# Performance work log

Measured on AMD Instinct MI355X. Metric: run time of the kernel, lower is better.

The kernel has to match this reference:

```python
import jax, jax.numpy as jnp
import numpy as np

IN_FT = 256
OUT_FT = 256


def setup_inputs() -> dict:
    key = jax.random.key(0)
    k1, k2, k3 = jax.random.split(key, 3)
    B, N = 4, 4096
    seq = jax.random.normal(k1, (B, N, IN_FT), dtype=jnp.float32)
    adj = jax.random.uniform(k2, (B, N, N), dtype=jnp.float32)
    # Xavier-uniform fc weight [out_ft, in_ft], bias zeros
    limit = float(np.sqrt(6.0 / (IN_FT + OUT_FT)))
    W = jax.random.uniform(k3, (OUT_FT, IN_FT), minval=-limit, maxval=limit, dtype=jnp.float32)
    b = jnp.zeros((OUT_FT,), dtype=jnp.float32)
    alpha = jnp.array(0.25, dtype=jnp.float32)  # PReLU shared parameter
    return {"seq": seq, "adj": adj, "W": W, "b": b, "alpha": alpha}


def reference(seq, adj, W, b, alpha):
    # Linear projection: [B, N, out_ft]
    h = jnp.einsum("bni,oi->bno", seq, W) + b
    # Neighbor aggregation (dense bmm path): [B, N, N] @ [B, N, out_ft]
    h = jnp.einsum("bnm,bmo->bno", adj, h)
    # PReLU with shared alpha
    return jnp.where(h > 0, h, alpha * h)
```

## Files before the change

### kernel.cpp

```cpp
#include <hip/hip_runtime.h>
#include <hip/hip_bf16.h>

#define NSEQ 4096
#define FT 256
#define BK 64
#define BKB 128
#define NTB (NSEQ / BKB)

typedef __attribute__((ext_vector_type(8))) short bf16x8;
typedef __attribute__((ext_vector_type(4))) float f32x4;

__device__ __forceinline__ ushort f2bf(float f) {
  __hip_bfloat16 h = __float2bfloat16(f);
  return *reinterpret_cast<const ushort*>(&h);
}

__device__ __forceinline__ int swz(int row, int byteInRow) {
  return row * 128 + (byteInRow ^ ((row & 7) << 4));
}

__device__ __forceinline__ void mma_step(const char* lAp, const char* lBp,
                                         int lane, int wm, int wn,
                                         f32x4 acc[2][4]) {
  const int r16 = lane & 15;
  const int g16 = (lane >> 4) * 16;
#pragma unroll
  for (int kk = 0; kk < 2; ++kk) {
    const int kb = kk * 64 + g16;
    bf16x8 a[2], b[4];
#pragma unroll
    for (int mi = 0; mi < 2; ++mi) {
      const int row = wm * 32 + mi * 16 + r16;
      a[mi] = *reinterpret_cast<const bf16x8*>(lAp + swz(row, kb));
    }
#pragma unroll
    for (int ni = 0; ni < 4; ++ni) {
      const int row = wn * 64 + ni * 16 + r16;
      b[ni] = *reinterpret_cast<const bf16x8*>(lBp + swz(row, kb));
    }
#pragma unroll
    for (int mi = 0; mi < 2; ++mi)
#pragma unroll
      for (int ni = 0; ni < 4; ++ni)
        acc[mi][ni] = __builtin_amdgcn_mfma_f32_16x16x32_bf16(a[mi], b[ni],
                                                             acc[mi][ni], 0, 0, 0);
  }
}

__global__ __launch_bounds__(512) void linear_kernel(
    const float* __restrict__ seq, const float* __restrict__ W,
    const float* __restrict__ bias, ushort* __restrict__ hT) {
  __shared__ __align__(16) ushort lA[2][64 * 64];
  __shared__ __align__(16) ushort lB[2][256 * 64];

  const int tid = threadIdx.x;
  const int lane = tid & 63;
  const int wid = tid >> 6;
  const int wm = wid >> 2, wn = wid & 3;
  const int m0 = blockIdx.x * 64;

  const int ar = tid >> 4, ac = tid & 15;

  f32x4 rA[2];
  f32x4 rB[8];

  auto gload = [&](int t) {
    const int k0 = t * BK;
#pragma unroll
    for (int p = 0; p < 2; ++p)
      rA[p] = *reinterpret_cast<const f32x4*>(
          seq + (size_t)(m0 + ar + p * 32) * FT + k0 + ac * 4);
#pragma unroll
    for (int p = 0; p < 8; ++p)
      rB[p] = *reinterpret_cast<const f32x4*>(
          W + (size_t)(ar + p * 32) * FT + k0 + ac * 4);
  };
  auto lwrite = [&](int buf) {
    char* lAp = (char*)lA[buf];
    char* lBp = (char*)lB[buf];
#pragma unroll
    for (int p = 0; p < 2; ++p) {
      ushort4 u = make_ushort4(f2bf(rA[p][0]), f2bf(rA[p][1]), f2bf(rA[p][2]), f2bf(rA[p][3]));
      *reinterpret_cast<ushort4*>(lAp + swz(ar + p * 32, ac * 8)) = u;
    }
#pragma unroll
    for (int p = 0; p < 8; ++p) {
      ushort4 u = make_ushort4(f2bf(rB[p][0]), f2bf(rB[p][1]), f2bf(rB[p][2]), f2bf(rB[p][3]));
      *reinterpret_cast<ushort4*>(lBp + swz(ar + p * 32, ac * 8)) = u;
    }
  };

  f32x4 acc[2][4];
  const f32x4 zero = {0.f, 0.f, 0.f, 0.f};
#pragma unroll
  for (int mi = 0; mi < 2; ++mi)
#pragma unroll
    for (int ni = 0; ni < 4; ++ni) acc[mi][ni] = zero;

  gload(0);
  lwrite(0);
  const int NTA = FT / BK;
  for (int t = 0; t < NTA; ++t) {
    const int cur = t & 1;
    __syncthreads();
    if (t + 1 < NTA) gload(t + 1);
    mma_step((const char*)lA[cur], (const char*)lB[cur], lane, wm, wn, acc);
    if (t + 1 < NTA) lwrite(cur ^ 1);
  }

#pragma unroll
  for (int mi = 0; mi < 2; ++mi) {
    const int grow = m0 + wm * 32 + mi * 16 + ((lane >> 4) << 2);
    const int batch = grow >> 12;
    const int n = grow & (NSEQ - 1);
#pragma unroll
    for (int ni = 0; ni < 4; ++ni) {
      const int o = wn * 64 + ni * 16 + (lane & 15);
      const float bo = bias[o];
      ushort4 u;
      u.x = f2bf(acc[mi][ni][0] + bo);
      u.y = f2bf(acc[mi][ni][1] + bo);
      u.z = f2bf(acc[mi][ni][2] + bo);
      u.w = f2bf(acc[mi][ni][3] + bo);
      *reinterpret_cast<ushort4*>(hT + (size_t)(batch * FT + o) * NSEQ + n) = u;
    }
  }
}

__global__ __launch_bounds__(512) void bmm_prelu_kernel(
    const float* __restrict__ adj, const ushort* __restrict__ hT,
    const float* __restrict__ alphaP, float* __restrict__ out) {
  __shared__ __align__(16) char smem[2 * 65536 + 2 * 16384];

  const int tid = threadIdx.x;
  const int lane = tid & 63;
  const int wid = tid >> 6;
  const int wm = wid >> 2, wn = wid & 3;

  const int bid = blockIdx.x;
  const int sbid = (bid & 7) * 32 + (bid >> 3);
  const int batch = sbid >> 6;
  const int m0 = (sbid & 63) * 64;

  const float* adjB = adj + (size_t)batch * NSEQ * NSEQ + (size_t)m0 * NSEQ;
  const ushort* hTB = hT + (size_t)batch * FT * NSEQ;

  auto lB = [&](int i) -> char* { return smem + i * 65536; };
  auto lA = [&](int i) -> char* { return smem + 131072 + i * 16384; };

  const int arow = tid >> 3, ac = tid & 7;
  const int bro = (lane >> 4);
  const int bhalf = (lane >> 3) & 1;
  f32x4 rS[4];

  f32x4 acc[2][4];
  const f32x4 zero = {0.f, 0.f, 0.f, 0.f};
#pragma unroll
  for (int mi = 0; mi < 2; ++mi)
#pragma unroll
    for (int ni = 0; ni < 4; ++ni) acc[mi][ni] = zero;

  auto issueA = [&](int t) {
    const int k0 = t * BKB;
#pragma unroll
    for (int q = 0; q < 4; ++q)
      rS[q] = *reinterpret_cast<const f32x4*>(
          adjB + (size_t)arow * NSEQ + k0 + ac * 16 + q * 4);
  };
  auto issueB = [&](int t, int ib) {
    const int k0 = t * BKB;
#pragma unroll
    for (int p = 0; p < 8; ++p) {
      const int grow = wid * 32 + p * 4 + bro;
      const int gsrc = (lane & 7) ^ (((p & 1) * 4 + bro) & 7);
      const ushort* gp = hTB + (size_t)grow * NSEQ + k0 + bhalf * 64 + gsrc * 8;
      char* lp = lB(ib) + wid * 8192 + p * 1024;
      __builtin_amdgcn_global_load_lds(
          (const __attribute__((address_space(1))) void*)gp,
          (__attribute__((address_space(3))) void*)lp, 16, 0, 0);
    }
  };
  auto writeA = [&](int ia) {
    char* lAp = lA(ia);
    const int half = ac >> 2;
#pragma unroll
    for (int q = 0; q < 4; ++q) {
      ushort4 u = make_ushort4(f2bf(rS[q][0]), f2bf(rS[q][1]),
                               f2bf(rS[q][2]), f2bf(rS[q][3]));
      const int gih = (((ac & 3) * 2 + (q >> 1)) ^ (arow & 7));
      *reinterpret_cast<ushort4*>(lAp + arow * 256 + half * 128 + gih * 16 +
                                  (q & 1) * 8) = u;
    }
  };
  auto mma32 = [&](const char* lAp, const char* lBp) {
    const int r16 = lane & 15;
    const int sub = lane >> 4;
#pragma unroll
    for (int kk = 0; kk < 4; ++kk) {
      const int half = kk >> 1;
      const int gih = (((kk & 1) * 4 + sub) ^ (r16 & 7));
      const int bofs = half * 128 + gih * 16;
      bf16x8 a[2], b[4];
#pragma unroll
      for (int mi = 0; mi < 2; ++mi) {
        const int row = wm * 32 + mi * 16 + r16;
        a[mi] = *reinterpret_cast<const bf16x8*>(lAp + row * 256 + bofs);
      }
#pragma unroll
      for (int ni = 0; ni < 4; ++ni) {
        const int row = wn * 64 + ni * 16 + r16;
        b[ni] = *reinterpret_cast<const bf16x8*>(lBp + row * 256 + bofs);
      }
#pragma unroll
      for (int mi = 0; mi < 2; ++mi)
#pragma unroll
        for (int ni = 0; ni < 4; ++ni)
          acc[mi][ni] = __builtin_amdgcn_mfma_f32_16x16x32_bf16(
              a[mi], b[ni], acc[mi][ni], 0, 0, 0);
    }
  };

  issueA(0);
  __builtin_amdgcn_sched_barrier(0);
  issueB(0, 0);
  __builtin_amdgcn_sched_barrier(0);
  asm volatile("s_waitcnt vmcnt(8)" ::: "memory");
  __builtin_amdgcn_sched_barrier(0);
  writeA(0);
  asm volatile("s_waitcnt vmcnt(0) lgkmcnt(0)" ::: "memory");
  __builtin_amdgcn_s_barrier();
  __builtin_amdgcn_sched_barrier(0);

  auto body = [&](int t, int cur) {
    issueA(t + 1);
    __builtin_amdgcn_sched_barrier(0);
    issueB(t + 1, cur ^ 1);
    __builtin_amdgcn_sched_barrier(0);
    __builtin_amdgcn_s_setprio(1);
    mma32(lA(cur), lB(cur));
    __builtin_amdgcn_s_setprio(0);
    asm volatile("s_waitcnt vmcnt(8)" ::: "memory");
    __builtin_amdgcn_sched_barrier(0);
    writeA(cur ^ 1);
    asm volatile("s_waitcnt vmcnt(0) lgkmcnt(0)" ::: "memory");
    __builtin_amdgcn_s_barrier();
    __builtin_amdgcn_sched_barrier(0);
  };

  for (int j = 0; j < 15; ++j) {
    body(2 * j, 0);
    body(2 * j + 1, 1);
  }
  body(30, 0);
  __builtin_amdgcn_s_setprio(1);
  mma32(lA(1), lB(1));
  __builtin_amdgcn_s_setprio(0);

  const float alpha = *alphaP;
  __syncthreads();
  float* lo = (float*)smem;
  const int PITCH = 264;
#pragma unroll
  for (int mi = 0; mi < 2; ++mi) {
    const int rbase = wm * 32 + mi * 16 + ((lane >> 4) << 2);
#pragma unroll
    for (int ni = 0; ni < 4; ++ni) {
      const int o = wn * 64 + ni * 16 + (lane & 15);
#pragma unroll
      for (int j = 0; j < 4; ++j) {
        float v = acc[mi][ni][j];
        v = v > 0.f ? v : alpha * v;
        lo[(rbase + j) * PITCH + o] = v;
      }
    }
  }
  __syncthreads();
  float* outB = out + ((size_t)batch * NSEQ + m0) * FT;
  const int r = tid >> 3, c8 = tid & 7;
#pragma unroll
  for (int k = 0; k < 8; ++k) {
    const int g = c8 + k * 8;
    f32x4 v = *reinterpret_cast<const f32x4*>(lo + r * PITCH + g * 4);
    __builtin_nontemporal_store(v, reinterpret_cast<f32x4*>(outB + (size_t)r * FT + g * 4));
  }
}

extern "C" void kernel_launch(void* const* d_in, const int* in_sizes, int n_in,
                              void* d_out, int out_size, void* d_ws, size_t ws_size,
                              hipStream_t stream) {
  const float* seq = (const float*)d_in[0];
  const float* adj = (const float*)d_in[1];
  const float* W = (const float*)d_in[2];
  const float* bias = (const float*)d_in[3];
  const float* alpha = (const float*)d_in[4];
  float* out = (float*)d_out;
  ushort* hT = (ushort*)d_ws;

  linear_kernel<<<256, 512, 0, stream>>>(seq, W, bias, hT);
  bmm_prelu_kernel<<<256, 512, 0, stream>>>(adj, hT, alpha, out);
}
```

Measured before the change: 83.63 us.

## Split B tile into half-K ring stages with finer-grained load/compute overlap

Replaces the double-buffered 128-wide B tile with a four-slot ring of 64-wide half tiles, so the second half of the next B tile is issued only after the first half of the current compute. Waits now use partial vmcnt counts and an extra mid-iteration barrier, which lets global-to-LDS loads overlap MFMA work more finely and stops draining all loads before each barrier. The B LDS layout changes to 128-byte rows with a new XOR swizzle. The cost is an extra barrier per iteration and reliance on exact waitcnt counts for correctness.

```diff
diff --git a/kernel.cpp b/kernel.cpp
--- a/kernel.cpp
+++ b/kernel.cpp
@@ -130,7 +130,7 @@
 __global__ __launch_bounds__(512) void bmm_prelu_kernel(
     const float* __restrict__ adj, const ushort* __restrict__ hT,
     const float* __restrict__ alphaP, float* __restrict__ out) {
-  __shared__ __align__(16) char smem[2 * 65536 + 2 * 16384];
+  __shared__ __align__(16) char smem[4 * 32768 + 2 * 16384];
 
   const int tid = threadIdx.x;
   const int lane = tid & 63;
@@ -145,12 +145,13 @@
   const float* adjB = adj + (size_t)batch * NSEQ * NSEQ + (size_t)m0 * NSEQ;
   const ushort* hTB = hT + (size_t)batch * FT * NSEQ;
 
-  auto lB = [&](int i) -> char* { return smem + i * 65536; };
+  auto ring = [&](int i) -> char* { return smem + i * 32768; };
   auto lA = [&](int i) -> char* { return smem + 131072 + i * 16384; };
 
+  const int br = lane >> 3;
+  const int bgr = (lane & 7) ^ br;
   const int arow = tid >> 3, ac = tid & 7;
-  const int bro = (lane >> 4);
-  const int bhalf = (lane >> 3) & 1;
+
   f32x4 rS[4];
 
   f32x4 acc[2][4];
@@ -167,14 +168,13 @@
       rS[q] = *reinterpret_cast<const f32x4*>(
           adjB + (size_t)arow * NSEQ + k0 + ac * 16 + q * 4);
   };
-  auto issueB = [&](int t, int ib) {
-    const int k0 = t * BKB;
-#pragma unroll
-    for (int p = 0; p < 8; ++p) {
-      const int grow = wid * 32 + p * 4 + bro;
-      const int gsrc = (lane & 7) ^ (((p & 1) * 4 + bro) & 7);
-      const ushort* gp = hTB + (size_t)grow * NSEQ + k0 + bhalf * 64 + gsrc * 8;
-      char* lp = lB(ib) + wid * 8192 + p * 1024;
+  auto issueBh = [&](int t, int h, int s) {
+    const int k0 = t * BKB + h * 64;
+#pragma unroll
+    for (int p = 0; p < 4; ++p) {
+      const ushort* gp =
+          hTB + (size_t)(p * 64 + wid * 8 + br) * NSEQ + k0 + bgr * 8;
+      char* lp = ring(s) + p * 8192 + wid * 1024;
       __builtin_amdgcn_global_load_lds(
           (const __attribute__((address_space(1))) void*)gp,
           (__attribute__((address_space(3))) void*)lp, 16, 0, 0);
@@ -192,25 +192,21 @@
                                   (q & 1) * 8) = u;
     }
   };
-  auto mma32 = [&](const char* lAp, const char* lBp) {
+  auto compute_half = [&](int h, const char* lAp, const char* lBp) {
     const int r16 = lane & 15;
     const int sub = lane >> 4;
 #pragma unroll
-    for (int kk = 0; kk < 4; ++kk) {
-      const int half = kk >> 1;
-      const int gih = (((kk & 1) * 4 + sub) ^ (r16 & 7));
-      const int bofs = half * 128 + gih * 16;
+    for (int kk2 = 0; kk2 < 2; ++kk2) {
+      const int gih = ((kk2 * 4 + sub) ^ (r16 & 7));
       bf16x8 a[2], b[4];
 #pragma unroll
-      for (int mi = 0; mi < 2; ++mi) {
-        const int row = wm * 32 + mi * 16 + r16;
-        a[mi] = *reinterpret_cast<const bf16x8*>(lAp + row * 256 + bofs);
-      }
-#pragma unroll
-      for (int ni = 0; ni < 4; ++ni) {
-        const int row = wn * 64 + ni * 16 + r16;
-        b[ni] = *reinterpret_cast<const bf16x8*>(lBp + row * 256 + bofs);
-      }
+      for (int mi = 0; mi < 2; ++mi)
+        a[mi] = *reinterpret_cast<const bf16x8*>(
+            lAp + (wm * 32 + mi * 16 + r16) * 256 + h * 128 + gih * 16);
+#pragma unroll
+      for (int ni = 0; ni < 4; ++ni)
+        b[ni] = *reinterpret_cast<const bf16x8*>(
+            lBp + (wn * 64 + ni * 16 + r16) * 128 + gih * 16);
 #pragma unroll
       for (int mi = 0; mi < 2; ++mi)
 #pragma unroll
@@ -220,41 +216,51 @@
     }
   };
 
+  issueBh(0, 0, 0);
   issueA(0);
-  __builtin_amdgcn_sched_barrier(0);
-  issueB(0, 0);
-  __builtin_amdgcn_sched_barrier(0);
-  asm volatile("s_waitcnt vmcnt(8)" ::: "memory");
-  __builtin_amdgcn_sched_barrier(0);
+  issueBh(0, 1, 1);
+  asm volatile("s_waitcnt vmcnt(4)" ::: "memory");
   writeA(0);
-  asm volatile("s_waitcnt vmcnt(0) lgkmcnt(0)" ::: "memory");
+  asm volatile("s_waitcnt lgkmcnt(0)" ::: "memory");
   __builtin_amdgcn_s_barrier();
   __builtin_amdgcn_sched_barrier(0);
 
-  auto body = [&](int t, int cur) {
+  auto body = [&](int t, int cur, int s0, int s1, int sI0, int sI1) {
+    issueBh(t + 1, 0, sI0);
     issueA(t + 1);
+    __builtin_amdgcn_s_setprio(1);
+    compute_half(0, lA(cur), ring(s0));
+    __builtin_amdgcn_s_setprio(0);
+    asm volatile("s_waitcnt vmcnt(8)" ::: "memory");
+    __builtin_amdgcn_s_barrier();
     __builtin_amdgcn_sched_barrier(0);
-    issueB(t + 1, cur ^ 1);
+    issueBh(t + 1, 1, sI1);
+    __builtin_amdgcn_s_setprio(1);
+    compute_half(1, lA(cur), ring(s1));
+    __builtin_amdgcn_s_setprio(0);
+    asm volatile("s_waitcnt vmcnt(4)" ::: "memory");
+    writeA(cur ^ 1);
+    asm volatile("s_waitcnt lgkmcnt(0)" ::: "memory");
+    __builtin_amdgcn_s_barrier();
+    __builtin_amdgcn_sched_barrier(0);
+  };
+
+  for (int j = 0; j < 15; ++j) {
+    body(2 * j, 0, 0, 1, 2, 3);
+    body(2 * j + 1, 1, 2, 3, 0, 1);
+  }
+  body(30, 0, 0, 1, 2, 3);
+  {
+    __builtin_amdgcn_s_setprio(1);
+    compute_half(0, lA(1), ring(2));
+    __builtin_amdgcn_s_setprio(0);
+    asm volatile("s_waitcnt vmcnt(0)" ::: "memory");
+    __builtin_amdgcn_s_barrier();
     __builtin_amdgcn_sched_barrier(0);
     __builtin_amdgcn_s_setprio(1);
-    mma32(lA(cur), lB(cur));
+    compute_half(1, lA(1), ring(3));
     __builtin_amdgcn_s_setprio(0);
-    asm volatile("s_waitcnt vmcnt(8)" ::: "memory");
-    __builtin_amdgcn_sched_barrier(0);
-    writeA(cur ^ 1);
-    asm volatile("s_waitcnt vmcnt(0) lgkmcnt(0)" ::: "memory");
-    __builtin_amdgcn_s_barrier();
-    __builtin_amdgcn_sched_barrier(0);
-  };
-
-  for (int j = 0; j < 15; ++j) {
-    body(2 * j, 0);
-    body(2 * j + 1, 1);
-  }
-  body(30, 0);
-  __builtin_amdgcn_s_setprio(1);
-  mma32(lA(1), lB(1));
-  __builtin_amdgcn_s_setprio(0);
+  }
 
   const float alpha = *alphaP;
   __syncthreads();
```

After: 85.30 us. 1.02x slower.
